# Kernel tuning notes

Measured on AMD Instinct MI355X. Metric: run time of the kernel, lower is better.

The kernel has to match this reference:

```python
import jax, jax.numpy as jnp
import numpy as np

N = 100000
E = 3200000
CH_IN = 128
HID = 128
CH_OUT = 3


def setup_inputs() -> dict:
    key = jax.random.key(0)
    ks = jax.random.split(key, 16)
    def lin(kw, fan_in, fan_out):
        bound = 1.0 / np.sqrt(fan_in)
        kw1, kw2 = jax.random.split(kw)
        W = jax.random.uniform(kw1, (fan_in, fan_out), jnp.float32, -bound, bound)
        b = jax.random.uniform(kw2, (fan_out,), jnp.float32, -bound, bound)
        return W, b
    x = jax.random.normal(ks[0], (N, CH_IN), jnp.float32)
    edge_index = jax.random.randint(ks[1], (2, E), 0, N, jnp.int64)
    W1, b1 = lin(ks[2], CH_IN, HID)
    W2, b2 = lin(ks[3], HID, HID)
    lw1, lb1 = lin(ks[4], HID, HID)
    lw2, lb2 = lin(ks[5], HID, HID)
    lw3, lb3 = lin(ks[6], HID, HID)
    lw4, lb4 = lin(ks[7], HID, CH_OUT)
    return {"x": x, "edge_index": edge_index,
            "W1": W1, "b1": b1, "W2": W2, "b2": b2,
            "lw1": lw1, "lb1": lb1, "lw2": lw2, "lb2": lb2,
            "lw3": lw3, "lb3": lb3, "lw4": lw4, "lb4": lb4}


def gcn_conv(x, W, b, src, dst, n_nodes):
    xw = x @ W  # [N, H]
    ew = jnp.ones(src.shape[0], x.dtype)
    deg = jax.ops.segment_sum(ew, dst, num_segments=n_nodes) + 2.0  # +2 from improved self-loop
    dinv = jnp.where(deg > 0, jax.lax.rsqrt(deg), 0.0)
    norm = dinv[src] * dinv[dst]  # [E]
    agg = jax.ops.segment_sum(xw[src] * norm[:, None], dst, num_segments=n_nodes)
    # self-loop contribution: weight 2 * dinv[i]^2 * xw[i]
    agg = agg + xw * (2.0 * dinv * dinv)[:, None]
    return agg + b


def reference(x, edge_index, W1, b1, W2, b2, lw1, lb1, lw2, lb2, lw3, lb3, lw4, lb4):
    src, dst = edge_index[0], edge_index[1]
    n = x.shape[0]
    h = jnp.tanh(gcn_conv(x, W1, b1, src, dst, n))
    h = jnp.tanh(gcn_conv(h, W2, b2, src, dst, n))
    # dropout in eval mode = identity
    h = jnp.tanh(h @ lw1 + lb1)
    h = jnp.tanh(h @ lw2 + lb2)
    h = jnp.tanh(h @ lw3 + lb3)
    return h @ lw4 + lb4
```

## Files before the change

### kernel.cpp

```cpp
#include <hip/hip_runtime.h>

typedef __attribute__((ext_vector_type(8))) short short8;
typedef __attribute__((ext_vector_type(4))) float floatx4;
typedef __attribute__((ext_vector_type(4))) unsigned int uintx4;
typedef unsigned int uint32;

__device__ inline float b2f(unsigned short u) {
    union { uint32 i; float f; } x; x.i = ((uint32)u) << 16; return x.f;
}
__device__ inline float bl(uint32 v) {
    union { uint32 i; float f; } x; x.i = v << 16; return x.f;
}
__device__ inline float bh(uint32 v) {
    union { uint32 i; float f; } x; x.i = v & 0xffff0000u; return x.f;
}
__device__ inline unsigned short f2b(float f) {
    union { float f; uint32 u; } x; x.f = f;
    uint32 r = x.u + 0x7fffu + ((x.u >> 16) & 1u);
    return (unsigned short)(r >> 16);
}
__device__ inline float fast_tanh(float x) {
    float ax = __builtin_fabsf(x);
    float t = __builtin_amdgcn_exp2f(-2.8853900817779268f * ax);
    float r = (1.0f - t) * __builtin_amdgcn_rcpf(1.0f + t);
    return __builtin_copysignf(r, x);
}


#define CHUNK 8192
#define MAXBK 512
#define CAP   8704

__global__ __launch_bounds__(512, 2) void scatterb_k(const int* __restrict__ eidx,
                                                     uint32* __restrict__ bkt_cur,
                                                     uint32* __restrict__ packed, int E) {
    __shared__ uint32 hist[MAXBK];
    __shared__ uint32 ssum[MAXBK];
    __shared__ uint32 hsc[MAXBK];
    __shared__ uint32 gbase[MAXBK];
    __shared__ uint32 lcur[MAXBK];
    __shared__ uint32 stage[CHUNK];
    __shared__ unsigned short stgb[CHUNK];
    int t = threadIdx.x;
    int cbase = blockIdx.x * CHUNK;
    int n = E - cbase; if (n > CHUNK) n = CHUNK;

    hist[t] = 0;
    __syncthreads();
    int dreg[CHUNK / 512];
    int nt = 0;
    for (int i = t; i < n; i += 512) {
        int d = eidx[E + cbase + i];
        dreg[nt++] = d;
        atomicAdd(&hist[d >> 8], 1u);
    }
    __syncthreads();
    uint32 v = hist[t];
    ssum[t] = v;
    __syncthreads();
    for (int off = 1; off < MAXBK; off <<= 1) {
        uint32 x = (t >= off) ? ssum[t - off] : 0;
        __syncthreads();
        ssum[t] += x;
        __syncthreads();
    }
    uint32 excl = ssum[t] - v;
    hsc[t] = excl;
    lcur[t] = excl;
    if (v) gbase[t] = atomicAdd(&bkt_cur[t], v);
    __syncthreads();
    nt = 0;
    for (int i = t; i < n; i += 512) {
        int s = eidx[cbase + i];
        int d = dreg[nt++];
        int b = d >> 8;
        uint32 pos = atomicAdd(&lcur[b], 1u);
        stage[pos] = ((uint32)s << 8) | (uint32)(d & 255);
        stgb[pos] = (unsigned short)b;
    }
    __syncthreads();
    for (int i = t; i < n; i += 512) {
        int b = stgb[i];
        packed[gbase[b] + (i - hsc[b])] = stage[i];
    }
}

__global__ __launch_bounds__(256) void buildb_k(const uint32* __restrict__ packed,
                                                const uint32* __restrict__ bkt_cur,
                                                int* __restrict__ rowp,
                                                int* __restrict__ rowe,
                                                float* __restrict__ dinv,
                                                int* __restrict__ csr, int N) {
    __shared__ uint32 cnt[256];
    __shared__ uint32 incl[256];
    __shared__ uint32 cur[256];
    int t = threadIdx.x;
    int b = blockIdx.x;
    uint32 base = (uint32)b * CAP;
    uint32 size = bkt_cur[b] - base;
    int node0 = b << 8;

    cnt[t] = 0;
    __syncthreads();
    for (uint32 i = t; i < size; i += 256)
        atomicAdd(&cnt[packed[base + i] & 255u], 1u);
    __syncthreads();
    uint32 v = cnt[t];
    incl[t] = v;
    __syncthreads();
    for (int off = 1; off < 256; off <<= 1) {
        uint32 x = (t >= off) ? incl[t - off] : 0;
        __syncthreads();
        incl[t] += x;
        __syncthreads();
    }
    uint32 loc = incl[t] - v;
    cur[t] = loc;
    int node = node0 + t;
    if (node < N) {
        dinv[node] = rsqrtf((float)v + 2.0f);
        rowp[node] = (int)(base + loc);
        rowe[node] = (int)(base + loc + v);
    }
    __syncthreads();
    for (uint32 i = t; i < size; i += 256) {
        uint32 p = packed[base + i];
        uint32 pos = atomicAdd(&cur[p & 255u], 1u);
        csr[base + pos] = (int)(p >> 8);
    }
}


__global__ __launch_bounds__(256) void prep_w5_k(const float* __restrict__ w0,
                                                 const float* __restrict__ w1,
                                                 const float* __restrict__ w2,
                                                 const float* __restrict__ w3,
                                                 const float* __restrict__ w4,
                                                 unsigned short* __restrict__ Wt_hi,
                                                 unsigned short* __restrict__ Wt_lo,
                                                 uint32* __restrict__ bkt_cur) {
    if (blockIdx.x < 2) {
        int idx = blockIdx.x * 256 + threadIdx.x;
        bkt_cur[idx] = (uint32)idx * CAP;
    }
    int t = blockIdx.x * 256 + threadIdx.x;
    int widx = t >> 11;
    int f8 = t & 2047;
    const float* W;
    switch (widx) {
        case 0: W = w0; break;
        case 1: W = w1; break;
        case 2: W = w2; break;
        case 3: W = w3; break;
        default: W = w4; break;
    }
    int ct = f8 >> 8, kc = (f8 >> 6) & 3, quad = (f8 >> 4) & 3, r = f8 & 15;
    int c = ct * 16 + r;
    int kbase = kc * 32 + quad * 8;
    short8 hi8, lo8;
#pragma unroll
    for (int j = 0; j < 8; ++j) {
        float w = W[(kbase + j) * 128 + c];
        unsigned short h = f2b(w);
        hi8[j] = (short)h;
        lo8[j] = (short)f2b(w - b2f(h));
    }
    *(short8*)(Wt_hi + widx * 16384 + f8 * 8) = hi8;
    *(short8*)(Wt_lo + widx * 16384 + f8 * 8) = lo8;
}


template <int ASRC>
__global__ __launch_bounds__(256, 4) void gemm_z_k(
    const void* __restrict__ Asrc,
    const unsigned short* __restrict__ Wt_hi,
    const unsigned short* __restrict__ Wt_lo,
    const float* __restrict__ dinv,
    unsigned short* __restrict__ out, int N) {
    int tid = threadIdx.x;
    int wave = tid >> 6, lane = tid & 63;
    int quad = lane >> 4, r = lane & 15;
    int m32 = blockIdx.x * 128 + wave * 32;

    short8 af[2][4];
#pragma unroll
    for (int s = 0; s < 2; ++s) {
        int rowA = m32 + s * 16 + r;
        if (rowA >= N) rowA = N - 1;
        if (ASRC == 0) {
            const float4* Af = (const float4*)Asrc;
#pragma unroll
            for (int kc = 0; kc < 4; ++kc) {
                float4 p0 = Af[((size_t)rowA * 128 + kc * 32 + quad * 8) >> 2];
                float4 p1 = Af[(((size_t)rowA * 128 + kc * 32 + quad * 8) >> 2) + 1];
                short8 a;
                a[0] = (short)f2b(p0.x); a[1] = (short)f2b(p0.y);
                a[2] = (short)f2b(p0.z); a[3] = (short)f2b(p0.w);
                a[4] = (short)f2b(p1.x); a[5] = (short)f2b(p1.y);
                a[6] = (short)f2b(p1.z); a[7] = (short)f2b(p1.w);
                af[s][kc] = a;
            }
        } else {
            const short* Ap = (const short*)Asrc;
#pragma unroll
            for (int kc = 0; kc < 4; ++kc)
                af[s][kc] = *(const short8*)(Ap + (size_t)rowA * 128 + kc * 32 + quad * 8);
        }
    }

    float dv[2][4];
#pragma unroll
    for (int s = 0; s < 2; ++s)
#pragma unroll
        for (int reg = 0; reg < 4; ++reg) {
            int i = m32 + s * 16 + quad * 4 + reg;
            dv[s][reg] = dinv[i < N ? i : N - 1];
        }

    const short8* WhF = (const short8*)Wt_hi + lane;
    const short8* WlF = (const short8*)Wt_lo + lane;

#pragma unroll
    for (int ct = 0; ct < 8; ++ct) {
        int n = ct * 16 + r;
        floatx4 a0 = {0.f, 0.f, 0.f, 0.f}, a1 = {0.f, 0.f, 0.f, 0.f};
#pragma unroll
        for (int kc = 0; kc < 4; ++kc) {
            short8 bh8 = WhF[(ct * 4 + kc) << 6];
            a0 = __builtin_amdgcn_mfma_f32_16x16x32_bf16(af[0][kc], bh8, a0, 0, 0, 0);
            a1 = __builtin_amdgcn_mfma_f32_16x16x32_bf16(af[1][kc], bh8, a1, 0, 0, 0);
            short8 bl8 = WlF[(ct * 4 + kc) << 6];
            a0 = __builtin_amdgcn_mfma_f32_16x16x32_bf16(af[0][kc], bl8, a0, 0, 0, 0);
            a1 = __builtin_amdgcn_mfma_f32_16x16x32_bf16(af[1][kc], bl8, a1, 0, 0, 0);
        }
#pragma unroll
        for (int reg = 0; reg < 4; ++reg) {
            int i0 = m32 + quad * 4 + reg;
            if (i0 < N) out[(size_t)i0 * 128 + n] = f2b(a0[reg] * dv[0][reg]);
            int i1 = m32 + 16 + quad * 4 + reg;
            if (i1 < N) out[(size_t)i1 * 128 + n] = f2b(a1[reg] * dv[1][reg]);
        }
    }
}


#define LSTR 136

__global__ __launch_bounds__(256, 2) void mlp_fused_k(
    const unsigned short* __restrict__ H,
    const unsigned short* __restrict__ WH,
    const unsigned short* __restrict__ WL,
    const float* __restrict__ lb1, const float* __restrict__ lb2,
    const float* __restrict__ lb3,
    const float* __restrict__ W4, const float* __restrict__ b4,
    float* __restrict__ out, int N) {
    __shared__ __align__(16) unsigned short wbuf[16384];
    __shared__ __align__(16) unsigned short tile[4][32 * LSTR];
    __shared__ float w4s[384];
    int tid = threadIdx.x;
    if (tid < 192) { w4s[tid] = W4[tid]; w4s[tid + 192] = W4[tid + 192]; }

    int wave = tid >> 6, lane = tid & 63;
    int quad = lane >> 4, r = lane & 15;
    unsigned short* T = tile[wave];
    int m32 = blockIdx.x * 128 + wave * 32;

    short8 af[2][4];
    const short* Hp = (const short*)H;
#pragma unroll
    for (int s = 0; s < 2; ++s) {
        int rowA = m32 + s * 16 + r;
        if (rowA >= N) rowA = N - 1;
#pragma unroll
        for (int kc = 0; kc < 4; ++kc)
            af[s][kc] = *(const short8*)(Hp + (size_t)rowA * 128 + kc * 32 + quad * 8);
    }

    const float* biases[3] = {lb1, lb2, lb3};
#pragma unroll
    for (int L = 0; L < 3; ++L) {
        const float* bias = biases[L];
        float bvv[8];
#pragma unroll
        for (int ct = 0; ct < 8; ++ct) bvv[ct] = bias[ct * 16 + r];
#pragma unroll
        for (int hf = 0; hf < 2; ++hf) {
            __syncthreads();
            {
                const uintx4* sh = (const uintx4*)(WH + L * 16384 + hf * 8192);
                const uintx4* sl = (const uintx4*)(WL + L * 16384 + hf * 8192);
                uintx4* dh = (uintx4*)wbuf;
                uintx4* dl = (uintx4*)(wbuf + 8192);
#pragma unroll
                for (int it = 0; it < 4; ++it) dh[tid + it * 256] = sh[tid + it * 256];
#pragma unroll
                for (int it = 0; it < 4; ++it) dl[tid + it * 256] = sl[tid + it * 256];
            }
            __syncthreads();
            const short8* whF = (const short8*)wbuf + lane;
            const short8* wlF = (const short8*)(wbuf + 8192) + lane;
#pragma unroll
            for (int c2 = 0; c2 < 4; ++c2) {
                int ct = hf * 4 + c2;
                int n = ct * 16 + r;
                floatx4 a0 = {0.f, 0.f, 0.f, 0.f}, a1 = {0.f, 0.f, 0.f, 0.f};
#pragma unroll
                for (int kc = 0; kc < 4; ++kc) {
                    short8 bh8 = whF[(c2 * 4 + kc) << 6];
                    a0 = __builtin_amdgcn_mfma_f32_16x16x32_bf16(af[0][kc], bh8, a0, 0, 0, 0);
                    a1 = __builtin_amdgcn_mfma_f32_16x16x32_bf16(af[1][kc], bh8, a1, 0, 0, 0);
                    short8 bl8 = wlF[(c2 * 4 + kc) << 6];
                    a0 = __builtin_amdgcn_mfma_f32_16x16x32_bf16(af[0][kc], bl8, a0, 0, 0, 0);
                    a1 = __builtin_amdgcn_mfma_f32_16x16x32_bf16(af[1][kc], bl8, a1, 0, 0, 0);
                }
                float bv = bvv[ct];
#pragma unroll
                for (int reg = 0; reg < 4; ++reg) {
                    int lrow = quad * 4 + reg;
                    T[lrow * LSTR + n] = f2b(fast_tanh(a0[reg] + bv));
                    T[(lrow + 16) * LSTR + n] = f2b(fast_tanh(a1[reg] + bv));
                }
            }
        }
        if (L < 2) {
#pragma unroll
            for (int s = 0; s < 2; ++s)
#pragma unroll
                for (int kc = 0; kc < 4; ++kc)
                    af[s][kc] = *(const short8*)&T[(s * 16 + r) * LSTR + kc * 32 + quad * 8];
        }
    }

    int lrow = lane & 31;
    int halfc = lane >> 5;
    float a0 = 0.f, a1 = 0.f, a2 = 0.f;
#pragma unroll
    for (int c8 = 0; c8 < 8; ++c8) {
        int cbase = halfc * 64 + c8 * 8;
        short8 hv = *(const short8*)&T[lrow * LSTR + cbase];
#pragma unroll
        for (int j = 0; j < 8; ++j) {
            float xv = b2f((unsigned short)hv[j]);
            int ch = cbase + j;
            a0 = fmaf(xv, w4s[ch * 3 + 0], a0);
            a1 = fmaf(xv, w4s[ch * 3 + 1], a1);
            a2 = fmaf(xv, w4s[ch * 3 + 2], a2);
        }
    }
    a0 += __shfl_xor(a0, 32);
    a1 += __shfl_xor(a1, 32);
    a2 += __shfl_xor(a2, 32);
    if (halfc == 0) {
        int i = m32 + lrow;
        if (i < N) {
            out[(size_t)i * 3 + 0] = a0 + b4[0];
            out[(size_t)i * 3 + 1] = a1 + b4[1];
            out[(size_t)i * 3 + 2] = a2 + b4[2];
        }
    }
}


__global__ __launch_bounds__(256) void agg_full_k(
    const uint32* __restrict__ z, const int* __restrict__ rowp,
    const int* __restrict__ rowe, const int* __restrict__ csr,
    const float* __restrict__ dinv, const float* __restrict__ bias,
    uint32* __restrict__ out, int N) {
    int lane = threadIdx.x & 63;
    int i = blockIdx.x * 4 + (threadIdx.x >> 6);
    if (i >= N) return;
    int start = rowp[i], end = rowe[i];
    const uint32* zl = z + lane;
    float a0 = 0.f, a1 = 0.f;
    for (int e = start; e < end; e += 64) {
        int cnt = end - e;
        if (cnt > 64) cnt = 64;
        int s = (lane < cnt) ? csr[e + lane] : N;
        int mp = (cnt + 15) & ~15;
        for (int m = 0; m < mp; m += 16) {
            uint32 v[16];
#pragma unroll
            for (int p = 0; p < 16; ++p) {
                int sj = __shfl(s, m + p);
                v[p] = zl[(size_t)sj << 6];
            }
#pragma unroll
            for (int p = 0; p < 16; ++p) {
                a0 += bl(v[p]);
                a1 += bh(v[p]);
            }
        }
    }
    uint32 vi = zl[(size_t)i << 6];
    a0 += 2.f * bl(vi);
    a1 += 2.f * bh(vi);
    float di = dinv[i];
    float2 bv = ((const float2*)bias)[lane];
    float h0 = fast_tanh(fmaf(di, a0, bv.x));
    float h1 = fast_tanh(fmaf(di, a1, bv.y));
    out[((size_t)i << 6) + lane] = (uint32)f2b(h0) | ((uint32)f2b(h1) << 16);
}

extern "C" void kernel_launch(void* const* d_in, const int* in_sizes, int n_in,
                              void* d_out, int out_size, void* d_ws, size_t ws_size,
                              hipStream_t stream) {
    const float* x   = (const float*)d_in[0];
    const int* eidx  = (const int*)d_in[1];
    const float* W1  = (const float*)d_in[2];
    const float* b1  = (const float*)d_in[3];
    const float* W2  = (const float*)d_in[4];
    const float* b2  = (const float*)d_in[5];
    const float* lw1 = (const float*)d_in[6];
    const float* lb1 = (const float*)d_in[7];
    const float* lw2 = (const float*)d_in[8];
    const float* lb2 = (const float*)d_in[9];
    const float* lw3 = (const float*)d_in[10];
    const float* lb3 = (const float*)d_in[11];
    const float* lw4 = (const float*)d_in[12];
    const float* lb4 = (const float*)d_in[13];
    float* out = (float*)d_out;

    const int N = in_sizes[0] / 128;
    const int E = in_sizes[1] / 2;

    char* p = (char*)d_ws;
    auto alloc = [&](size_t bytes) -> void* {
        void* q = (void*)p;
        p += (bytes + 255) & ~(size_t)255;
        return q;
    };
    const int NBK = (N + 255) >> 8;
    float* dinv      = (float*)alloc((size_t)N * 4);
    int* rowp        = (int*)alloc((size_t)N * 4);
    int* rowe        = (int*)alloc((size_t)N * 4);
    uint32* bkt_cur  = (uint32*)alloc(MAXBK * 4);
    int* csr         = (int*)alloc((size_t)NBK * CAP * 4);
    unsigned short* Wt_hi = (unsigned short*)alloc(5 * 16384 * 2);
    unsigned short* Wt_lo = (unsigned short*)alloc(5 * 16384 * 2);
    unsigned short* bufA  = (unsigned short*)alloc((size_t)(N + 1) * 128 * 2);
    unsigned short* bufB  = (unsigned short*)alloc((size_t)(N + 1) * 128 * 2);
    uint32* packed = (uint32*)bufA;

    const int MB4 = (N + 127) / 128;
    const int AB  = (N + 3) / 4;
    const int NCH = (E + CHUNK - 1) / CHUNK;

    hipMemsetAsync(bufA + (size_t)N * 128, 0, 256, stream);
    prep_w5_k<<<40, 256, 0, stream>>>(W1, W2, lw1, lw2, lw3, Wt_hi, Wt_lo, bkt_cur);
    scatterb_k<<<NCH, 512, 0, stream>>>(eidx, bkt_cur, packed, E);
    buildb_k<<<NBK, 256, 0, stream>>>(packed, bkt_cur, rowp, rowe, dinv, csr, N);

    const unsigned short* WH = Wt_hi;
    const unsigned short* WL = Wt_lo;

    gemm_z_k<0><<<MB4, 256, 0, stream>>>(x, WH + 0 * 16384, WL + 0 * 16384, dinv, bufA, N);
    agg_full_k<<<AB, 256, 0, stream>>>((const uint32*)bufA, rowp, rowe, csr, dinv, b1,
                                       (uint32*)bufB, N);
    gemm_z_k<1><<<MB4, 256, 0, stream>>>(bufB, WH + 1 * 16384, WL + 1 * 16384, dinv, bufA, N);
    agg_full_k<<<AB, 256, 0, stream>>>((const uint32*)bufA, rowp, rowe, csr, dinv, b2,
                                       (uint32*)bufB, N);
    mlp_fused_k<<<MB4, 256, 0, stream>>>(bufB, WH + 2 * 16384, WL + 2 * 16384,
                                         lb1, lb2, lb3, lw4, lb4, out, N);
}
```

Before: 455.3 us.

## Fold weight prep into CSR build, use wave-shuffle scans, add nontemporal agg accesses

Weight bf16 hi/lo splitting moves into the first 40 blocks of buildb_k and bkt_cur is reset with a memset instead of a separate kernel. The zero pad row is written inside gemm_z_k, which removes one launch and one memset. Block-wide shared-memory Hillis-Steele scans in scatterb_k and buildb_k become wave shuffle scans with one cross-wave step, which cuts many barriers. The first aggregation pass uses nontemporal loads for CSR indices and nontemporal stores for its output, aiming to keep the gathered z rows in cache.

```diff
diff --git a/kernel.cpp b/kernel.cpp
--- a/kernel.cpp
+++ b/kernel.cpp
@@ -35,10 +35,10 @@
                                                      uint32* __restrict__ bkt_cur,
                                                      uint32* __restrict__ packed, int E) {
     __shared__ uint32 hist[MAXBK];
-    __shared__ uint32 ssum[MAXBK];
     __shared__ uint32 hsc[MAXBK];
     __shared__ uint32 gbase[MAXBK];
     __shared__ uint32 lcur[MAXBK];
+    __shared__ uint32 wsum[8];
     __shared__ uint32 stage[CHUNK];
     __shared__ unsigned short stgb[CHUNK];
     int t = threadIdx.x;
@@ -56,18 +56,22 @@
     }
     __syncthreads();
     uint32 v = hist[t];
-    ssum[t] = v;
-    __syncthreads();
-    for (int off = 1; off < MAXBK; off <<= 1) {
-        uint32 x = (t >= off) ? ssum[t - off] : 0;
-        __syncthreads();
-        ssum[t] += x;
-        __syncthreads();
-    }
-    uint32 excl = ssum[t] - v;
+    uint32 x = v;
+    int lane = t & 63;
+#pragma unroll
+    for (int off = 1; off < 64; off <<= 1) {
+        uint32 y = __shfl_up(x, off);
+        if (lane >= off) x += y;
+    }
+    if (lane == 63) wsum[t >> 6] = x;
+    __syncthreads();
+    uint32 pre = 0;
+#pragma unroll
+    for (int w = 0; w < 8; ++w) pre += (w < (t >> 6)) ? wsum[w] : 0;
+    uint32 excl = x + pre - v;
     hsc[t] = excl;
     lcur[t] = excl;
-    if (v) gbase[t] = atomicAdd(&bkt_cur[t], v);
+    if (v) gbase[t] = (uint32)t * CAP + atomicAdd(&bkt_cur[t], v);
     __syncthreads();
     nt = 0;
     for (int i = t; i < n; i += 512) {
@@ -85,19 +89,54 @@
     }
 }
 
+
 __global__ __launch_bounds__(256) void buildb_k(const uint32* __restrict__ packed,
                                                 const uint32* __restrict__ bkt_cur,
                                                 int* __restrict__ rowp,
                                                 int* __restrict__ rowe,
                                                 float* __restrict__ dinv,
-                                                int* __restrict__ csr, int N) {
+                                                int* __restrict__ csr, int N,
+                                                const float* __restrict__ w0,
+                                                const float* __restrict__ w1,
+                                                const float* __restrict__ w2,
+                                                const float* __restrict__ w3,
+                                                const float* __restrict__ w4,
+                                                unsigned short* __restrict__ Wt_hi,
+                                                unsigned short* __restrict__ Wt_lo) {
     __shared__ uint32 cnt[256];
-    __shared__ uint32 incl[256];
     __shared__ uint32 cur[256];
+    __shared__ uint32 wsum4[4];
     int t = threadIdx.x;
     int b = blockIdx.x;
+
+    if (b < 40) {
+        int widx = b >> 3;
+        int f8 = ((b & 7) << 8) | t;
+        const float* W;
+        switch (widx) {
+            case 0: W = w0; break;
+            case 1: W = w1; break;
+            case 2: W = w2; break;
+            case 3: W = w3; break;
+            default: W = w4; break;
+        }
+        int ct = f8 >> 8, kc = (f8 >> 6) & 3, quad = (f8 >> 4) & 3, r = f8 & 15;
+        int c = ct * 16 + r;
+        int kbase = kc * 32 + quad * 8;
+        short8 hi8, lo8;
+#pragma unroll
+        for (int j = 0; j < 8; ++j) {
+            float w = W[(kbase + j) * 128 + c];
+            unsigned short h = f2b(w);
+            hi8[j] = (short)h;
+            lo8[j] = (short)f2b(w - b2f(h));
+        }
+        *(short8*)(Wt_hi + widx * 16384 + f8 * 8) = hi8;
+        *(short8*)(Wt_lo + widx * 16384 + f8 * 8) = lo8;
+    }
+
     uint32 base = (uint32)b * CAP;
-    uint32 size = bkt_cur[b] - base;
+    uint32 size = bkt_cur[b];
     int node0 = b << 8;
 
     cnt[t] = 0;
@@ -106,15 +145,19 @@
         atomicAdd(&cnt[packed[base + i] & 255u], 1u);
     __syncthreads();
     uint32 v = cnt[t];
-    incl[t] = v;
-    __syncthreads();
-    for (int off = 1; off < 256; off <<= 1) {
-        uint32 x = (t >= off) ? incl[t - off] : 0;
-        __syncthreads();
-        incl[t] += x;
-        __syncthreads();
-    }
-    uint32 loc = incl[t] - v;
+    uint32 x = v;
+    int lane = t & 63;
+#pragma unroll
+    for (int off = 1; off < 64; off <<= 1) {
+        uint32 y = __shfl_up(x, off);
+        if (lane >= off) x += y;
+    }
+    if (lane == 63) wsum4[t >> 6] = x;
+    __syncthreads();
+    uint32 pre = 0;
+#pragma unroll
+    for (int w = 0; w < 4; ++w) pre += (w < (t >> 6)) ? wsum4[w] : 0;
+    uint32 loc = x + pre - v;
     cur[t] = loc;
     int node = node0 + t;
     if (node < N) {
@@ -128,45 +171,6 @@
         uint32 pos = atomicAdd(&cur[p & 255u], 1u);
         csr[base + pos] = (int)(p >> 8);
     }
-}
-
-
-__global__ __launch_bounds__(256) void prep_w5_k(const float* __restrict__ w0,
-                                                 const float* __restrict__ w1,
-                                                 const float* __restrict__ w2,
-                                                 const float* __restrict__ w3,
-                                                 const float* __restrict__ w4,
-                                                 unsigned short* __restrict__ Wt_hi,
-                                                 unsigned short* __restrict__ Wt_lo,
-                                                 uint32* __restrict__ bkt_cur) {
-    if (blockIdx.x < 2) {
-        int idx = blockIdx.x * 256 + threadIdx.x;
-        bkt_cur[idx] = (uint32)idx * CAP;
-    }
-    int t = blockIdx.x * 256 + threadIdx.x;
-    int widx = t >> 11;
-    int f8 = t & 2047;
-    const float* W;
-    switch (widx) {
-        case 0: W = w0; break;
-        case 1: W = w1; break;
-        case 2: W = w2; break;
-        case 3: W = w3; break;
-        default: W = w4; break;
-    }
-    int ct = f8 >> 8, kc = (f8 >> 6) & 3, quad = (f8 >> 4) & 3, r = f8 & 15;
-    int c = ct * 16 + r;
-    int kbase = kc * 32 + quad * 8;
-    short8 hi8, lo8;
-#pragma unroll
-    for (int j = 0; j < 8; ++j) {
-        float w = W[(kbase + j) * 128 + c];
-        unsigned short h = f2b(w);
-        hi8[j] = (short)h;
-        lo8[j] = (short)f2b(w - b2f(h));
-    }
-    *(short8*)(Wt_hi + widx * 16384 + f8 * 8) = hi8;
-    *(short8*)(Wt_lo + widx * 16384 + f8 * 8) = lo8;
 }
 
 
@@ -178,6 +182,9 @@
     const float* __restrict__ dinv,
     unsigned short* __restrict__ out, int N) {
     int tid = threadIdx.x;
+    if (blockIdx.x == 0 && tid < 64) {
+        ((uint32*)out)[(size_t)N * 64 + tid] = 0;
+    }
     int wave = tid >> 6, lane = tid & 63;
     int quad = lane >> 4, r = lane & 15;
     int m32 = blockIdx.x * 128 + wave * 32;
@@ -361,6 +368,7 @@
 }
 
 
+template <int NT>
 __global__ __launch_bounds__(256) void agg_full_k(
     const uint32* __restrict__ z, const int* __restrict__ rowp,
     const int* __restrict__ rowe, const int* __restrict__ csr,
@@ -375,7 +383,12 @@
     for (int e = start; e < end; e += 64) {
         int cnt = end - e;
         if (cnt > 64) cnt = 64;
-        int s = (lane < cnt) ? csr[e + lane] : N;
+        int s;
+        if (lane < cnt) {
+            s = NT ? __builtin_nontemporal_load(&csr[e + lane]) : csr[e + lane];
+        } else {
+            s = N;
+        }
         int mp = (cnt + 15) & ~15;
         for (int m = 0; m < mp; m += 16) {
             uint32 v[16];
@@ -398,7 +411,12 @@
     float2 bv = ((const float2*)bias)[lane];
     float h0 = fast_tanh(fmaf(di, a0, bv.x));
     float h1 = fast_tanh(fmaf(di, a1, bv.y));
-    out[((size_t)i << 6) + lane] = (uint32)f2b(h0) | ((uint32)f2b(h1) << 16);
+    uint32 pv = (uint32)f2b(h0) | ((uint32)f2b(h1) << 16);
+    if (NT) {
+        __builtin_nontemporal_store(pv, &out[((size_t)i << 6) + lane]);
+    } else {
+        out[((size_t)i << 6) + lane] = pv;
+    }
 }
 
 extern "C" void kernel_launch(void* const* d_in, const int* in_sizes, int n_in,
@@ -445,20 +463,20 @@
     const int AB  = (N + 3) / 4;
     const int NCH = (E + CHUNK - 1) / CHUNK;
 
-    hipMemsetAsync(bufA + (size_t)N * 128, 0, 256, stream);
-    prep_w5_k<<<40, 256, 0, stream>>>(W1, W2, lw1, lw2, lw3, Wt_hi, Wt_lo, bkt_cur);
+    hipMemsetAsync(bkt_cur, 0, MAXBK * 4, stream);
     scatterb_k<<<NCH, 512, 0, stream>>>(eidx, bkt_cur, packed, E);
-    buildb_k<<<NBK, 256, 0, stream>>>(packed, bkt_cur, rowp, rowe, dinv, csr, N);
+    buildb_k<<<NBK, 256, 0, stream>>>(packed, bkt_cur, rowp, rowe, dinv, csr, N,
+                                      W1, W2, lw1, lw2, lw3, Wt_hi, Wt_lo);
 
     const unsigned short* WH = Wt_hi;
     const unsigned short* WL = Wt_lo;
 
     gemm_z_k<0><<<MB4, 256, 0, stream>>>(x, WH + 0 * 16384, WL + 0 * 16384, dinv, bufA, N);
-    agg_full_k<<<AB, 256, 0, stream>>>((const uint32*)bufA, rowp, rowe, csr, dinv, b1,
-                                       (uint32*)bufB, N);
+    agg_full_k<1><<<AB, 256, 0, stream>>>((const uint32*)bufA, rowp, rowe, csr, dinv, b1,
+                                          (uint32*)bufB, N);
     gemm_z_k<1><<<MB4, 256, 0, stream>>>(bufB, WH + 1 * 16384, WL + 1 * 16384, dinv, bufA, N);
-    agg_full_k<<<AB, 256, 0, stream>>>((const uint32*)bufA, rowp, rowe, csr, dinv, b2,
-                                       (uint32*)bufB, N);
+    agg_full_k<0><<<AB, 256, 0, stream>>>((const uint32*)bufA, rowp, rowe, csr, dinv, b2,
+                                          (uint32*)bufB, N);
     mlp_fused_k<<<MB4, 256, 0, stream>>>(bufB, WH + 2 * 16384, WL + 2 * 16384,
                                          lb1, lb2, lb3, lw4, lb4, out, N);
 }
```

New measurement: 454.8 us. Within noise of the previous version (-0.1%).
